# Performance work log

Measured on AMD Instinct MI355X. Metric: run time of the kernel, lower is better.

## Reference

```python
import jax, jax.numpy as jnp
import numpy as np

NUM_CAPSULE = 32
DIM_CAPSULE = 32
ROUTINGS = 3
T_EPSILON = 1e-7


def setup_inputs() -> dict:
    key = jax.random.key(0)
    k1, k2 = jax.random.split(key)
    x = jax.random.normal(k1, (64, 1024, 256), dtype=jnp.float32)
    # xavier_normal_ on [1, 256, 32*32]: std = sqrt(2/(fan_in+fan_out)) = sqrt(2/(256+1024))
    std = np.sqrt(2.0 / (256 + NUM_CAPSULE * DIM_CAPSULE)).astype(np.float32)
    W = jax.random.normal(k2, (1, 256, NUM_CAPSULE * DIM_CAPSULE), dtype=jnp.float32) * std
    return {"x": x, "W": W}


def _squash(v, eps):
    # x / sqrt(sum(x^2) + eps)  (note: not the classic squash; faithful to source)
    s = jnp.sum(v * v, axis=-1, keepdims=True)
    return v / jnp.sqrt(s + eps)


def reference(x, W):
    B, N_in, _ = x.shape
    # u_hat: [B, num_capsule, input_num_capsule, dim_capsule]
    u_hat = jnp.matmul(x, W).reshape(B, N_in, NUM_CAPSULE, DIM_CAPSULE)
    u_hat = jnp.transpose(u_hat, (0, 2, 1, 3))
    b = jnp.zeros(u_hat.shape[:3], dtype=u_hat.dtype)  # [B, num, n_in]
    outputs = None
    for i in range(ROUTINGS):
        # original: softmax over the num_capsule axis (dim=2 after permute(0,2,1))
        c = jax.nn.softmax(b, axis=1)  # [B, num, n_in]
        outputs = _squash(jnp.einsum('bij,bijk->bik', c, u_hat), T_EPSILON)  # [B, num, dim]
        if i < ROUTINGS - 1:
            b = jnp.einsum('bik,bijk->bij', outputs, u_hat)
    return outputs
```

## Files before the change

### kernel.cpp

```cpp
#include <hip/hip_runtime.h>
#include <cstdint>
#include <cstddef>

#define BATCH 64
#define NIN   1024
#define CIN   256
#define NC    32
#define NJC   16
#define JCH   64
#define T_EPS 1e-7f
#define CT_S  72
#define XT_SS 68

typedef __attribute__((ext_vector_type(8))) short short8;
typedef __attribute__((ext_vector_type(4))) float floatx4;

__device__ __forceinline__ unsigned short bf16rne(float f) {
  unsigned int u = __float_as_uint(f);
  u += 0x7FFFu + ((u >> 16) & 1u);
  return (unsigned short)(u >> 16);
}
__device__ __forceinline__ float bf2f(unsigned short h) {
  return __uint_as_float(((unsigned int)h) << 16);
}

__global__ __launch_bounds__(256) void k_convert(const float* __restrict__ x,
                                                 unsigned short* __restrict__ xb,
                                                 unsigned short* __restrict__ xbT,
                                                 float* __restrict__ y0p) {
  const int jc = blockIdx.x, b = blockIdx.y, t = threadIdx.x;
  __shared__ unsigned short xsT[CIN * XT_SS];
  const size_t base = ((size_t)(b * NIN + jc * JCH)) * CIN;
  float acc = 0.f;
  #pragma unroll 8
  for (int j = 0; j < JCH; ++j) {
    float v = x[base + (size_t)j * CIN + t];
    acc += v;
    unsigned short h = bf16rne(v);
    xb[base + (size_t)j * CIN + t] = h;
    xsT[t * XT_SS + j] = h;
  }
  y0p[(b * NJC + jc) * CIN + t] = acc;
  __syncthreads();
  ushort4* dstv = (ushort4*)(xbT + (size_t)(b * NJC + jc) * (CIN * JCH));
  #pragma unroll
  for (int it = 0; it < 16; ++it) {
    int f = it * 256 + t;
    int c = f >> 4, j4 = f & 15;
    dstv[f] = *(const ushort4*)&xsT[c * XT_SS + j4 * 4];
  }
}

template <int MODE>
__global__ __launch_bounds__(256) void k_post(const void* __restrict__ yin,
                                              const float* __restrict__ W,
                                              unsigned short* __restrict__ wtout,
                                              float* __restrict__ outg) {
  const int i = blockIdx.x, b = blockIdx.y, t = threadIdx.x;
  __shared__ float Wl[CIN][36];
  __shared__ float ys[CIN];
  __shared__ float sred[8][32];
  __shared__ float os[NC];
  const float4* W4 = (const float4*)W;
  #pragma unroll
  for (int q = 0; q < 8; ++q) {
    int f = q * 256 + t;
    int c = f >> 3, k4 = f & 7;
    float4 v = W4[c * (NC * 8) + i * 8 + k4];
    *(float4*)&Wl[c][k4 * 4] = v;
  }
  float a = 0.f;
  if (MODE == 0) {
    const float* y0p = (const float*)yin;
    #pragma unroll
    for (int p = 0; p < NJC; ++p) a += y0p[(b * NJC + p) * CIN + t];
    a *= (1.f / 32.f);
  } else {
    const unsigned short* yp = (const unsigned short*)yin;
    #pragma unroll
    for (int p = 0; p < NJC; ++p)
      a += bf2f(yp[(((size_t)(b * NJC + p)) * NC + i) * CIN + t]);
  }
  ys[t] = a;
  __syncthreads();
  {
    const int k = t & 31, g = t >> 5;
    float ps = 0.f;
    #pragma unroll
    for (int cc = 0; cc < 32; ++cc) {
      int c = g * 32 + cc;
      ps += ys[c] * Wl[c][k];
    }
    sred[g][k] = ps;
  }
  __syncthreads();
  const int k = t & 31;
  float s = 0.f;
  #pragma unroll
  for (int g = 0; g < 8; ++g) s += sred[g][k];
  float s2 = s * s;
  #pragma unroll
  for (int m = 1; m < 32; m <<= 1) s2 += __shfl_xor(s2, m);
  float o = s * rsqrtf(s2 + T_EPS);
  if (MODE == 2) {
    if (t < 32) outg[((size_t)b * NC + i) * 32 + t] = o;
  } else {
    if (t < 32) os[t] = o;
    __syncthreads();
    const int rot = ((t >> 3) & 7) * 4;
    float acc = 0.f;
    #pragma unroll
    for (int kkk = 0; kkk < 32; ++kkk) {
      int kk = (kkk + rot) & 31;
      acc += Wl[t][kk] * os[kk];
    }
    wtout[((size_t)b * NC + i) * CIN + t] = bf16rne(acc);
  }
}

__global__ __launch_bounds__(256, 4) void k_fused(const unsigned short* __restrict__ xb,
                                                  const unsigned short* __restrict__ xbT,
                                                  const unsigned short* __restrict__ wt,
                                                  unsigned short* __restrict__ ypart) {
  const int jc = blockIdx.x, b = blockIdx.y, t = threadIdx.x;
  const int w = t >> 6, l16 = t & 15, q = (t >> 4) & 3;
  __shared__ unsigned short cT[NC * CT_S];
  const int jloc = w * 16 + l16;
  const unsigned short* xrow =
      xb + ((size_t)(b * NIN) + (size_t)jc * JCH + jloc) * CIN;
  const unsigned short* wrow = wt + (size_t)b * NC * CIN;
  floatx4 accA0 = {0.f, 0.f, 0.f, 0.f}, accA1 = {0.f, 0.f, 0.f, 0.f};
  #pragma unroll
  for (int ks = 0; ks < 8; ++ks) {
    short8 bx = *(const short8*)(xrow + ks * 32 + q * 8);
    short8 a0 = *(const short8*)(wrow + (size_t)l16 * CIN + ks * 32 + q * 8);
    short8 a1 = *(const short8*)(wrow + (size_t)(16 + l16) * CIN + ks * 32 + q * 8);
    accA0 = __builtin_amdgcn_mfma_f32_16x16x32_bf16(a0, bx, accA0, 0, 0, 0);
    accA1 = __builtin_amdgcn_mfma_f32_16x16x32_bf16(a1, bx, accA1, 0, 0, 0);
  }
  {
    float m = accA0[0];
    #pragma unroll
    for (int r = 1; r < 4; ++r) m = fmaxf(m, accA0[r]);
    #pragma unroll
    for (int r = 0; r < 4; ++r) m = fmaxf(m, accA1[r]);
    m = fmaxf(m, __shfl_xor(m, 16));
    m = fmaxf(m, __shfl_xor(m, 32));
    float e0[4], e1[4], s = 0.f;
    #pragma unroll
    for (int r = 0; r < 4; ++r) {
      e0[r] = __expf(accA0[r] - m);
      e1[r] = __expf(accA1[r] - m);
      s += e0[r] + e1[r];
    }
    s += __shfl_xor(s, 16);
    s += __shfl_xor(s, 32);
    float rs = 1.f / s;
    #pragma unroll
    for (int r = 0; r < 4; ++r) {
      cT[(q * 4 + r) * CT_S + jloc]      = bf16rne(e0[r] * rs);
      cT[(16 + q * 4 + r) * CT_S + jloc] = bf16rne(e1[r] * rs);
    }
  }
  __syncthreads();
  const int cw = w * 64;
  const unsigned short* xTb = xbT + (size_t)(b * NJC + jc) * (CIN * JCH);
  floatx4 accB[2][4];
  #pragma unroll
  for (int h = 0; h < 2; ++h)
    #pragma unroll
    for (int ct = 0; ct < 4; ++ct) accB[h][ct] = (floatx4){0.f, 0.f, 0.f, 0.f};
  #pragma unroll
  for (int ks = 0; ks < 2; ++ks) {
    short8 ca0 = *(const short8*)&cT[l16 * CT_S + ks * 32 + q * 8];
    short8 ca1 = *(const short8*)&cT[(16 + l16) * CT_S + ks * 32 + q * 8];
    #pragma unroll
    for (int ct = 0; ct < 4; ++ct) {
      short8 xf = *(const short8*)(xTb + (size_t)(cw + ct * 16 + l16) * JCH + ks * 32 + q * 8);
      accB[0][ct] = __builtin_amdgcn_mfma_f32_16x16x32_bf16(ca0, xf, accB[0][ct], 0, 0, 0);
      accB[1][ct] = __builtin_amdgcn_mfma_f32_16x16x32_bf16(ca1, xf, accB[1][ct], 0, 0, 0);
    }
  }
  unsigned short* yo = ypart + ((size_t)(b * NJC + jc)) * NC * CIN;
  #pragma unroll
  for (int h = 0; h < 2; ++h)
    #pragma unroll
    for (int ct = 0; ct < 4; ++ct)
      #pragma unroll
      for (int r = 0; r < 4; ++r) {
        int i = h * 16 + q * 4 + r;
        int c = cw + ct * 16 + l16;
        yo[i * CIN + c] = bf16rne(accB[h][ct][r]);
      }
}

extern "C" void kernel_launch(void* const* d_in, const int* in_sizes, int n_in,
                              void* d_out, int out_size, void* d_ws, size_t ws_size,
                              hipStream_t stream) {
  (void)in_sizes; (void)n_in; (void)out_size; (void)ws_size;
  const float* x = (const float*)d_in[0];
  const float* W = (const float*)d_in[1];
  float* out = (float*)d_out;
  char* ws = (char*)d_ws;
  unsigned short* xbuf  = (unsigned short*)ws;
  unsigned short* xbufT = (unsigned short*)(ws + (32ull << 20));
  unsigned short* wtb   = (unsigned short*)(ws + (64ull << 20));
  unsigned short* ypart = (unsigned short*)(ws + (65ull << 20));
  float*          y0p   = (float*)(ws + (81ull << 20));

  dim3 gfuse(NJC, BATCH);
  dim3 gpost(NC, BATCH);
  k_convert<<<gfuse, 256, 0, stream>>>(x, xbuf, xbufT, y0p);
  k_post<0><<<gpost, 256, 0, stream>>>(y0p, W, wtb, nullptr);
  k_fused<<<gfuse, 256, 0, stream>>>(xbuf, xbufT, wtb, ypart);
  k_post<1><<<gpost, 256, 0, stream>>>(ypart, W, wtb, nullptr);
  k_fused<<<gfuse, 256, 0, stream>>>(xbuf, xbufT, wtb, ypart);
  k_post<2><<<gpost, 256, 0, stream>>>(ypart, W, nullptr, out);
}
```

Measured before the change: 172.2 us.

## Drop transposed x copy; stage x tile in swizzled LDS inside fused kernel

The convert kernel no longer writes a transposed bf16 copy of x; it now vectorizes loads and stores with float4 and reduces column sums through shared memory. The fused kernel loads its 64x256 bf16 x tile once into XOR-swizzled LDS and reads both row-major fragments and transposed column fragments from it, instead of reading x and its transpose from global memory. This removes a 32MB global write and its re-reads. In exchange it adds 32KB of LDS per block, which may lower occupancy, and a scalar gather of eight 16-bit LDS reads per transposed fragment.

```diff
diff --git a/kernel.cpp b/kernel.cpp
--- a/kernel.cpp
+++ b/kernel.cpp
@@ -10,7 +10,6 @@
 #define JCH   64
 #define T_EPS 1e-7f
 #define CT_S  72
-#define XT_SS 68
 
 typedef __attribute__((ext_vector_type(8))) short short8;
 typedef __attribute__((ext_vector_type(4))) float floatx4;
@@ -24,30 +23,39 @@
   return __uint_as_float(((unsigned int)h) << 16);
 }
 
+__device__ __forceinline__ int xsw(int j, int c) {
+  return j * 256 + ((((c >> 3) ^ (j & 7) ^ ((j >> 3) & 7)) << 3) | (c & 7));
+}
+
 __global__ __launch_bounds__(256) void k_convert(const float* __restrict__ x,
                                                  unsigned short* __restrict__ xb,
-                                                 unsigned short* __restrict__ xbT,
                                                  float* __restrict__ y0p) {
   const int jc = blockIdx.x, b = blockIdx.y, t = threadIdx.x;
-  __shared__ unsigned short xsT[CIN * XT_SS];
-  const size_t base = ((size_t)(b * NIN + jc * JCH)) * CIN;
-  float acc = 0.f;
-  #pragma unroll 8
-  for (int j = 0; j < JCH; ++j) {
-    float v = x[base + (size_t)j * CIN + t];
-    acc += v;
-    unsigned short h = bf16rne(v);
-    xb[base + (size_t)j * CIN + t] = h;
-    xsT[t * XT_SS + j] = h;
-  }
-  y0p[(b * NJC + jc) * CIN + t] = acc;
-  __syncthreads();
-  ushort4* dstv = (ushort4*)(xbT + (size_t)(b * NJC + jc) * (CIN * JCH));
-  #pragma unroll
-  for (int it = 0; it < 16; ++it) {
-    int f = it * 256 + t;
-    int c = f >> 4, j4 = f & 15;
-    dstv[f] = *(const ushort4*)&xsT[c * XT_SS + j4 * 4];
+  const int jj = t >> 6, c4 = t & 63;
+  __shared__ float4 red[4][64];
+  const float4* xg = (const float4*)(x + ((size_t)(b * NIN + jc * JCH)) * CIN);
+  ushort4* xo = (ushort4*)(xb + ((size_t)(b * NIN + jc * JCH)) * CIN);
+  float4 acc = make_float4(0.f, 0.f, 0.f, 0.f);
+  #pragma unroll
+  for (int jr = 0; jr < 16; ++jr) {
+    int j = jr * 4 + jj;
+    float4 v = xg[j * 64 + c4];
+    acc.x += v.x; acc.y += v.y; acc.z += v.z; acc.w += v.w;
+    ushort4 h;
+    h.x = bf16rne(v.x); h.y = bf16rne(v.y);
+    h.z = bf16rne(v.z); h.w = bf16rne(v.w);
+    xo[j * 64 + c4] = h;
+  }
+  red[jj][c4] = acc;
+  __syncthreads();
+  if (t < 64) {
+    float4 s = red[0][t];
+    #pragma unroll
+    for (int p = 1; p < 4; ++p) {
+      s.x += red[p][t].x; s.y += red[p][t].y;
+      s.z += red[p][t].z; s.w += red[p][t].w;
+    }
+    *(float4*)&y0p[(b * NJC + jc) * CIN + t * 4] = s;
   }
 }
 
@@ -119,20 +127,29 @@
 }
 
 __global__ __launch_bounds__(256, 4) void k_fused(const unsigned short* __restrict__ xb,
-                                                  const unsigned short* __restrict__ xbT,
                                                   const unsigned short* __restrict__ wt,
                                                   unsigned short* __restrict__ ypart) {
   const int jc = blockIdx.x, b = blockIdx.y, t = threadIdx.x;
   const int w = t >> 6, l16 = t & 15, q = (t >> 4) & 3;
+  __shared__ unsigned short xs[64 * 256];
   __shared__ unsigned short cT[NC * CT_S];
+  {
+    const short8* xg =
+        (const short8*)(xb + ((size_t)(b * NIN) + (size_t)jc * JCH) * CIN);
+    #pragma unroll
+    for (int it = 0; it < 8; ++it) {
+      int f = it * 256 + t;
+      int j = f >> 5, ch = f & 31;
+      *(short8*)&xs[xsw(j, ch * 8)] = xg[f];
+    }
+  }
   const int jloc = w * 16 + l16;
-  const unsigned short* xrow =
-      xb + ((size_t)(b * NIN) + (size_t)jc * JCH + jloc) * CIN;
   const unsigned short* wrow = wt + (size_t)b * NC * CIN;
   floatx4 accA0 = {0.f, 0.f, 0.f, 0.f}, accA1 = {0.f, 0.f, 0.f, 0.f};
+  __syncthreads();
   #pragma unroll
   for (int ks = 0; ks < 8; ++ks) {
-    short8 bx = *(const short8*)(xrow + ks * 32 + q * 8);
+    short8 bx = *(const short8*)&xs[xsw(jloc, ks * 32 + q * 8)];
     short8 a0 = *(const short8*)(wrow + (size_t)l16 * CIN + ks * 32 + q * 8);
     short8 a1 = *(const short8*)(wrow + (size_t)(16 + l16) * CIN + ks * 32 + q * 8);
     accA0 = __builtin_amdgcn_mfma_f32_16x16x32_bf16(a0, bx, accA0, 0, 0, 0);
@@ -164,7 +181,6 @@
   }
   __syncthreads();
   const int cw = w * 64;
-  const unsigned short* xTb = xbT + (size_t)(b * NJC + jc) * (CIN * JCH);
   floatx4 accB[2][4];
   #pragma unroll
   for (int h = 0; h < 2; ++h)
@@ -176,7 +192,11 @@
     short8 ca1 = *(const short8*)&cT[(16 + l16) * CT_S + ks * 32 + q * 8];
     #pragma unroll
     for (int ct = 0; ct < 4; ++ct) {
-      short8 xf = *(const short8*)(xTb + (size_t)(cw + ct * 16 + l16) * JCH + ks * 32 + q * 8);
+      const int c = cw + ct * 16 + l16;
+      short8 xf;
+      #pragma unroll
+      for (int e = 0; e < 8; ++e)
+        xf[e] = (short)xs[xsw(ks * 32 + q * 8 + e, c)];
       accB[0][ct] = __builtin_amdgcn_mfma_f32_16x16x32_bf16(ca0, xf, accB[0][ct], 0, 0, 0);
       accB[1][ct] = __builtin_amdgcn_mfma_f32_16x16x32_bf16(ca1, xf, accB[1][ct], 0, 0, 0);
     }
@@ -203,17 +223,16 @@
   float* out = (float*)d_out;
   char* ws = (char*)d_ws;
   unsigned short* xbuf  = (unsigned short*)ws;
-  unsigned short* xbufT = (unsigned short*)(ws + (32ull << 20));
-  unsigned short* wtb   = (unsigned short*)(ws + (64ull << 20));
-  unsigned short* ypart = (unsigned short*)(ws + (65ull << 20));
-  float*          y0p   = (float*)(ws + (81ull << 20));
+  unsigned short* wtb   = (unsigned short*)(ws + (32ull << 20));
+  unsigned short* ypart = (unsigned short*)(ws + (33ull << 20));
+  float*          y0p   = (float*)(ws + (49ull << 20));
 
   dim3 gfuse(NJC, BATCH);
   dim3 gpost(NC, BATCH);
-  k_convert<<<gfuse, 256, 0, stream>>>(x, xbuf, xbufT, y0p);
+  k_convert<<<gfuse, 256, 0, stream>>>(x, xbuf, y0p);
   k_post<0><<<gpost, 256, 0, stream>>>(y0p, W, wtb, nullptr);
-  k_fused<<<gfuse, 256, 0, stream>>>(xbuf, xbufT, wtb, ypart);
+  k_fused<<<gfuse, 256, 0, stream>>>(xbuf, wtb, ypart);
   k_post<1><<<gpost, 256, 0, stream>>>(ypart, W, wtb, nullptr);
-  k_fused<<<gfuse, 256, 0, stream>>>(xbuf, xbufT, wtb, ypart);
+  k_fused<<<gfuse, 256, 0, stream>>>(xbuf, wtb, ypart);
   k_post<2><<<gpost, 256, 0, stream>>>(ypart, W, nullptr, out);
 }
```

Measured after the change: 159.2 us. 1.08x faster.
